# Optimization experiments

Hardware: AMD Instinct MI355X
Metric: run time of the kernel (lower is better)

The kernel has to match this reference:

```python
import jax, jax.numpy as jnp
import numpy as np

MAX_CLUSTERS = 5
CLUSTER_SIZE_MAX = 3
K_HOP = 2
TAU = 1.0  # epoch=0 -> tau_init * decay^0 = 1.0
NEG = -1e9


def _logits(x, ctx, W1, b1, W2, b2):
    # x: [B,N,D], ctx: [B,H] -> logits [B,N] (selection_mlp, dropout=eval/identity)
    B, N, _ = x.shape
    h = jnp.concatenate([x, jnp.broadcast_to(ctx[:, None, :], (B, N, ctx.shape[-1]))], axis=-1)
    h = jax.nn.relu(h @ W1.T + b1)
    return (h @ W2.T + b2)[..., 0]


def _select(logits, cand, key):
    # Hard Gumbel-Softmax argmax over candidate nodes; zeros row if no candidates.
    any_c = cand.any(axis=-1, keepdims=True)
    ml = jnp.where(cand, logits, NEG)
    u = jax.random.uniform(key, logits.shape, dtype=logits.dtype)
    g = -jnp.log(-jnp.log(u + 1e-8) + 1e-8)
    idx = jnp.argmax((ml + g) / TAU, axis=-1)
    oh = jax.nn.one_hot(idx, logits.shape[-1], dtype=logits.dtype)
    return oh * any_c.astype(logits.dtype)


def _gru(seq, h0, Wih, Whh, bih, bhh):
    # torch nn.GRU single layer, batch_first; seq: [B,T,D], h0: [B,H] -> final hidden [B,H]
    def cell(h, xt):
        gi = xt @ Wih.T + bih
        gh = h @ Whh.T + bhh
        ir, iz, inn = jnp.split(gi, 3, axis=-1)
        hr, hz, hn = jnp.split(gh, 3, axis=-1)
        r = jax.nn.sigmoid(ir + hr)
        z = jax.nn.sigmoid(iz + hz)
        n = jnp.tanh(inn + r * hn)
        return (1.0 - z) * n + z * h, None
    h, _ = jax.lax.scan(cell, h0, jnp.swapaxes(seq, 0, 1))
    return h


def reference(x, adj, mask, W1, b1, W2, b2, Wc, bc, Wih, Whh, bih, bhh):
    B, N, D = x.shape
    key = jax.random.key(42)
    avail = mask.astype(bool)
    ctx = x.mean(axis=1) @ Wc.T + bc          # context_init  [B,H]
    h_gru = jnp.zeros_like(ctx)               # context_hidden
    assign = jnp.zeros((B, N, MAX_CLUSTERS), x.dtype)
    embs, hist = [], []
    for c in range(MAX_CLUSTERS):
        # logits are identical for every selection within this cluster (same x, same context)
        logits = _logits(x, ctx, W1, b1, W2, b2)  # [B,N]
        # seed selection (torch uses .item() -> selection is a constant index; no grad path)
        seed = jax.lax.stop_gradient(_select(logits, avail, jax.random.fold_in(key, 2 * c)))
        avail = avail & ~(seed > 0.5)
        # k-hop BFS from seed via adjacency matvecs
        reach = seed > 0.5
        cur = seed
        for _ in range(K_HOP):
            nb = jnp.einsum('bn,bnm->bm', cur, adj) > 0
            new = nb & ~reach
            reach = reach | nb
            cur = new.astype(x.dtype)
        member = seed
        for a in range(CLUSTER_SIZE_MAX - 1):
            cand = avail & reach
            sel = jax.lax.stop_gradient(_select(logits, cand, jax.random.fold_in(key, 2 * c + 1000 + a)))
            avail = avail & ~(sel > 0.5)
            member = member + sel
        assign = assign.at[:, :, c].set(member)
        cnt = member.sum(axis=-1, keepdims=True)
        emb = jnp.einsum('bn,bnd->bd', member, x) / jnp.maximum(cnt, 1.0)  # mean of member feats; 0 if empty
        embs.append(emb)
        hist.append(emb)
        # torch re-runs the GRU over the FULL cluster history each iteration, starting
        # from the previously updated hidden state (faithful to the original code)
        h_gru = _gru(jnp.stack(hist, axis=1), h_gru, Wih, Whh, bih, bhh)
        ctx = h_gru
    cluster_features = jnp.stack(embs, axis=1)               # [B,S,D]
    S = MAX_CLUSTERS
    cluster_adj = jnp.ones((B, S, S), x.dtype) - jnp.eye(S, dtype=x.dtype)[None]
    return cluster_features, cluster_adj, assign


def setup_inputs() -> dict:
    key = jax.random.key(0)
    ks = jax.random.split(key, 10)
    B, N, D, H = 16, 2048, 128, 64
    x = jax.random.normal(ks[0], (B, N, D), dtype=jnp.float32)
    # sparse symmetric binary adjacency, ~16 neighbors per node
    a = (jax.random.uniform(ks[1], (B, N, N)) < 0.004).astype(jnp.float32)
    adj = jnp.clip(a + jnp.swapaxes(a, 1, 2), 0.0, 1.0)
    adj = adj * (1.0 - jnp.eye(N, dtype=jnp.float32)[None])
    mask = jnp.ones((B, N), dtype=jnp.int32)
    s = 0.05
    return {
        'x': x, 'adj': adj, 'mask': mask,
        'W1': jax.random.normal(ks[2], (H, D + H)) * s, 'b1': jnp.zeros((H,)),
        'W2': jax.random.normal(ks[3], (1, H)) * s, 'b2': jnp.zeros((1,)),
        'Wc': jax.random.normal(ks[4], (H, D)) * s, 'bc': jnp.zeros((H,)),
        'Wih': jax.random.normal(ks[5], (3 * H, D)) * s,
        'Whh': jax.random.normal(ks[6], (3 * H, H)) * s,
        'bih': jnp.zeros((3 * H,)), 'bhh': jnp.zeros((3 * H,)),
    }
```

## Files before the change

kernel.cpp:

```cpp
#include <hip/hip_runtime.h>
#include <cfloat>
#include <cmath>

#define NB 2048
#define BB 16
#define DD 128
#define HH 64
#define MAXC 5
#define CSMAX 3
#define NT 1024

__device__ __forceinline__ unsigned rotl32(unsigned v, int d) {
  return (v << d) | (v >> (32 - d));
}

__device__ __forceinline__ void tf2x32(unsigned k0, unsigned k1, unsigned x0, unsigned x1,
                                       unsigned& o0, unsigned& o1) {
  unsigned ks2 = k0 ^ k1 ^ 0x1BD11BDAu;
  x0 += k0; x1 += k1;
#define RND(r) { x0 += x1; x1 = rotl32(x1, r); x1 ^= x0; }
  RND(13) RND(15) RND(26) RND(6)   x0 += k1;  x1 += ks2 + 1u;
  RND(17) RND(29) RND(16) RND(24)  x0 += ks2; x1 += k0 + 2u;
  RND(13) RND(15) RND(26) RND(6)   x0 += k0;  x1 += k1 + 3u;
  RND(17) RND(29) RND(16) RND(24)  x0 += k1;  x1 += ks2 + 4u;
  RND(13) RND(15) RND(26) RND(6)   x0 += ks2; x1 += k0 + 5u;
#undef RND
  o0 = x0; o1 = x1;
}

__device__ __forceinline__ float gumbel_for(unsigned k0, unsigned k1, unsigned idx) {
  unsigned o0, o1;
  tf2x32(k0, k1, 0u, idx, o0, o1);
  unsigned bits = o0 ^ o1;
  float u = __uint_as_float((bits >> 9) | 0x3f800000u) - 1.0f;
  float uu = u + 1e-8f;
  return -logf(-logf(uu) + 1e-8f);
}

__global__ __launch_bounds__(NT) void gvp_prep(
    const float* __restrict__ x, const float* __restrict__ W1,
    float* __restrict__ P, float* __restrict__ partial, float* __restrict__ gumb) {
  __shared__ __align__(16) float s_W1[HH][DD + 4];
  __shared__ float sp[8][DD];
  const int bid = blockIdx.x, tid = threadIdx.x;

  if (bid < 128) {
    for (int i = tid; i < HH * (DD / 4); i += NT) {
      int r = i >> 5, q = i & 31;
      *(float4*)&s_W1[r][q * 4] = *(const float4*)(W1 + (size_t)r * (DD + HH) + q * 4);
    }
    __syncthreads();
    const int jg = tid & 15, ng = tid >> 4;
    const int j0 = jg * 4;
    const size_t n0 = (size_t)bid * 256 + ng * 4;
    const float4* x4 = (const float4*)x;
    float acc[4][4];
#pragma unroll
    for (int i = 0; i < 4; i++)
#pragma unroll
      for (int q = 0; q < 4; q++) acc[i][q] = 0.f;
    for (int kq = 0; kq < 32; kq++) {
      float4 xv[4], wv[4];
#pragma unroll
      for (int i = 0; i < 4; i++) xv[i] = x4[(n0 + i) * 32 + kq];
#pragma unroll
      for (int q = 0; q < 4; q++) wv[q] = *(const float4*)&s_W1[j0 + q][kq * 4];
#pragma unroll
      for (int i = 0; i < 4; i++)
#pragma unroll
        for (int q = 0; q < 4; q++)
          acc[i][q] += xv[i].x * wv[q].x + xv[i].y * wv[q].y +
                       xv[i].z * wv[q].z + xv[i].w * wv[q].w;
    }
#pragma unroll
    for (int i = 0; i < 4; i++)
#pragma unroll
      for (int q = 0; q < 4; q++)
        P[(n0 + i) * HH + j0 + q] = acc[i][q];
  } else if (bid < 384) {
    const int bm = bid - 128;
    const int b = bm >> 4, chunk = bm & 15;
    const int d = tid & (DD - 1), part = tid >> 7;
    float acc = 0.f;
    const int base = chunk * 128 + part;
#pragma unroll
    for (int k = 0; k < 16; k++)
      acc += x[((size_t)b * NB + base + k * 8) * DD + d];
    sp[part][d] = acc;
    __syncthreads();
    if (tid < DD) {
      float m = 0.f;
#pragma unroll
      for (int p = 0; p < 8; p++) m += sp[p][tid];
      partial[((size_t)b * 16 + chunk) * DD + tid] = m;
    }
  } else {
    const int bg = bid - 384;
    const int base = (bg * NT + tid) * 4;
#pragma unroll
    for (int i = 0; i < 4; i++) {
      int idx = base + i;
      int sel = idx >> 15;
      int rem = idx & 32767;
      int c = sel / 3, s = sel - 3 * c;
      unsigned data = (s == 0) ? (unsigned)(2 * c) : (unsigned)(2 * c + 1000 + (s - 1));
      unsigned k0, k1;
      tf2x32(0u, 42u, 0u, data, k0, k1);
      gumb[idx] = gumbel_for(k0, k1, (unsigned)rem);
    }
  }
}

__global__ __launch_bounds__(NT, 4) void gvp_main(
    const float* __restrict__ x, const float* __restrict__ adj, const int* __restrict__ mask,
    const float* __restrict__ W1, const float* __restrict__ b1,
    const float* __restrict__ W2, const float* __restrict__ b2,
    const float* __restrict__ Wc, const float* __restrict__ bc,
    const float* __restrict__ Wih, const float* __restrict__ Whh,
    const float* __restrict__ bih, const float* __restrict__ bhh,
    const float* __restrict__ P, const float* __restrict__ partial,
    const float* __restrict__ gumb,
    float* __restrict__ out_feat, float* __restrict__ out_adjm, float* __restrict__ out_assign) {
  const int b = blockIdx.x;
  const int tid = threadIdx.x;

  __shared__ __align__(16) float s_logits[NB];
  __shared__ __align__(16) float s_gumb[2][NB];
  __shared__ unsigned char s_avail[NB], s_reach[NB], s_assignB[NB];
  __shared__ short s_list[128];
  __shared__ int s_cnt;
  __shared__ unsigned long long s_key[CSMAX];
  __shared__ __align__(16) float s_ctx[HH], s_q[HH];
  __shared__ __align__(16) float s_h[2][HH];
  __shared__ __align__(16) float s_hist[MAXC][DD];
  __shared__ __align__(16) float s_giAll[MAXC][3 * HH];
  __shared__ __align__(16) float s_Whh[3 * HH][HH + 4];
  __shared__ __align__(16) float s_W1c[HH][HH + 4];
  __shared__ __align__(16) float s_W2[HH];
  __shared__ float s_bhh[3 * HH], s_b1[HH];
  __shared__ __align__(16) float s_mean[DD];
  __shared__ float s_b2v;

  const size_t xb = (size_t)b * NB * DD;
  const float4* adj4 = (const float4*)(adj + (size_t)b * NB * NB);
  const float4* P4 = (const float4*)(P + (size_t)b * NB * HH);

  auto scanReduce = [&](float bv, int bi, int slot) {
#pragma unroll
    for (int off = 32; off; off >>= 1) {
      float ov = __shfl_down(bv, off);
      int oi = __shfl_down(bi, off);
      if (ov > bv || (ov == bv && oi < bi)) { bv = ov; bi = oi; }
    }
    if ((tid & 63) == 0 && bi < NB) {
      unsigned u = __float_as_uint(bv);
      u = (u & 0x80000000u) ? ~u : (u | 0x80000000u);
      unsigned long long key = ((unsigned long long)u << 32) | (unsigned)(~bi);
      atomicMax(&s_key[slot], key);
    }
  };
  auto decodeIdx = [](unsigned long long k) -> int {
    return k ? (int)(unsigned)(~(unsigned)k) : -1;
  };

  for (int i = tid; i < 3 * HH * (HH / 4); i += NT) {
    int r = i >> 4, q = i & 15;
    *(float4*)&s_Whh[r][q * 4] = *(const float4*)(Whh + (size_t)r * HH + q * 4);
  }
  {
    int r = tid >> 4, q = tid & 15;
    *(float4*)&s_W1c[r][q * 4] = *(const float4*)(W1 + (size_t)r * (DD + HH) + DD + q * 4);
  }
  if (tid < 3 * HH) s_bhh[tid] = bhh[tid];
  if (tid < HH) { s_W2[tid] = W2[tid]; s_b1[tid] = b1[tid]; s_h[0][tid] = 0.f; }
  if (tid == 0) s_b2v = b2[0];
#pragma unroll
  for (int r = 0; r < 2; r++) {
    int n = tid + r * NT;
    s_avail[n] = (mask[b * NB + n] != 0) ? 1 : 0;
    s_assignB[n] = 0;
  }
  if (tid < DD) {
    float m = 0.f;
#pragma unroll
    for (int k = 0; k < 16; k++) m += partial[((size_t)b * 16 + k) * DD + tid];
    s_mean[tid] = m * (1.0f / NB);
  }
  __syncthreads();
  if (tid < 4 * HH) {
    int row = tid >> 2, g = tid & 3;
    const float4* wr = (const float4*)(Wc + (size_t)row * DD) + g * 8;
    const float4* m4 = (const float4*)s_mean + g * 8;
    float s = 0.f;
#pragma unroll
    for (int i = 0; i < 8; i++) {
      float4 w = wr[i], m = m4[i];
      s += w.x * m.x + w.y * m.y + w.z * m.z + w.w * m.w;
    }
    s += __shfl_xor(s, 1);
    s += __shfl_xor(s, 2);
    if (g == 0) s_ctx[row] = s + bc[row];
  }
  __syncthreads();

  int hp = 0;

  for (int c = 0; c < MAXC; c++) {
    const float* g0p = gumb + ((size_t)(c * 3) * BB + b) * NB;
    const float4* g12 = (const float4*)(gumb + ((size_t)(c * 3 + 1 + (tid >> 9)) * BB + b) * NB);
    float4 gst = g12[tid & 511];
    const int n0 = tid, n1 = tid + NT;
    float gs0 = g0p[n0], gs1 = g0p[n1];
    ((float4*)s_gumb)[tid] = gst;
    if (tid < 4 * HH) {
      int row = tid >> 2, g = tid & 3;
      const float4* wr = (const float4*)&s_W1c[row][0] + g * 4;
      const float4* c4 = (const float4*)s_ctx + g * 4;
      float s = 0.f;
#pragma unroll
      for (int i = 0; i < 4; i++) {
        float4 w = wr[i], cc = c4[i];
        s += w.x * cc.x + w.y * cc.y + w.z * cc.z + w.w * cc.w;
      }
      s += __shfl_xor(s, 1);
      s += __shfl_xor(s, 2);
      if (g == 0) s_q[row] = s + s_b1[row];
    }
    if (tid < CSMAX) s_key[tid] = 0ull;
    if (tid == 0) s_cnt = 0;
    __syncthreads();

    {
      float l0 = s_b2v, l1 = s_b2v;
      const float4* p0 = P4 + (size_t)n0 * 16;
      const float4* p1 = P4 + (size_t)n1 * 16;
      const float4* q4 = (const float4*)s_q;
      const float4* w4 = (const float4*)s_W2;
#pragma unroll
      for (int qq = 0; qq < 16; qq += 4) {
        float4 A[4], Bv[4];
#pragma unroll
        for (int i = 0; i < 4; i++) { A[i] = p0[qq + i]; Bv[i] = p1[qq + i]; }
#pragma unroll
        for (int i = 0; i < 4; i++) {
          float4 qv = q4[qq + i], w = w4[qq + i];
          l0 += w.x * fmaxf(A[i].x + qv.x, 0.f) + w.y * fmaxf(A[i].y + qv.y, 0.f) +
                w.z * fmaxf(A[i].z + qv.z, 0.f) + w.w * fmaxf(A[i].w + qv.w, 0.f);
          l1 += w.x * fmaxf(Bv[i].x + qv.x, 0.f) + w.y * fmaxf(Bv[i].y + qv.y, 0.f) +
                w.z * fmaxf(Bv[i].z + qv.z, 0.f) + w.w * fmaxf(Bv[i].w + qv.w, 0.f);
        }
      }
      s_logits[n0] = l0;
      s_logits[n1] = l1;
      float bv = -FLT_MAX;
      int bi = NB;
      if (s_avail[n0]) { float y = l0 + gs0; if (y > bv) { bv = y; bi = n0; } }
      if (s_avail[n1]) { float y = l1 + gs1; if (y > bv || (y == bv && n1 < bi)) { bv = y; bi = n1; } }
      scanReduce(bv, bi, 0);
    }
    __syncthreads();

    const int seed = decodeIdx(s_key[0]);
    if (tid < 512) {
      if (seed >= 0) {
        float4 a = adj4[(size_t)seed * 512 + tid];
        int m = tid << 2;
        unsigned f0 = a.x > 0.f, f1 = a.y > 0.f, f2 = a.z > 0.f, f3 = a.w > 0.f;
        unsigned r = f0 | (f1 << 8) | (f2 << 16) | (f3 << 24);
        if ((seed >> 2) == tid) r |= 1u << ((seed & 3) * 8);
        ((unsigned*)s_reach)[tid] = r;
        if (f0 && m != seed)     { int p = atomicAdd(&s_cnt, 1); if (p < 128) s_list[p] = (short)m; }
        if (f1 && m + 1 != seed) { int p = atomicAdd(&s_cnt, 1); if (p < 128) s_list[p] = (short)(m + 1); }
        if (f2 && m + 2 != seed) { int p = atomicAdd(&s_cnt, 1); if (p < 128) s_list[p] = (short)(m + 2); }
        if (f3 && m + 3 != seed) { int p = atomicAdd(&s_cnt, 1); if (p < 128) s_list[p] = (short)(m + 3); }
      } else {
        ((unsigned*)s_reach)[tid] = 0u;
      }
    }
    __syncthreads();

    if (seed >= 0) {
      int cnt = min(s_cnt, 128);
      int m4 = tid & 511, rg = tid >> 9;
      bool a0 = false, a1 = false, a2 = false, a3 = false;
#pragma unroll
      for (int k = 0; k < 20; k++) {
        int li = rg + 2 * k;
        if (li < cnt) {
          int n = s_list[li];
          float4 a = adj4[(size_t)n * 512 + m4];
          a0 |= a.x > 0.f; a1 |= a.y > 0.f; a2 |= a.z > 0.f; a3 |= a.w > 0.f;
        }
      }
      for (int li = rg + 40; li < cnt; li += 2) {
        int n = s_list[li];
        float4 a = adj4[(size_t)n * 512 + m4];
        a0 |= a.x > 0.f; a1 |= a.y > 0.f; a2 |= a.z > 0.f; a3 |= a.w > 0.f;
      }
      int m = m4 << 2;
      if (a0) s_reach[m] = 1;
      if (a1) s_reach[m + 1] = 1;
      if (a2) s_reach[m + 2] = 1;
      if (a3) s_reach[m + 3] = 1;
    }
    __syncthreads();

    {
      float bv = -FLT_MAX;
      int bi = NB;
#pragma unroll
      for (int r = 0; r < 2; r++) {
        int n = tid + r * NT;
        if (s_avail[n] && s_reach[n] && n != seed) {
          float y = s_logits[n] + s_gumb[0][n];
          if (y > bv || (y == bv && n < bi)) { bv = y; bi = n; }
        }
      }
      scanReduce(bv, bi, 1);
    }
    __syncthreads();

    const int w1i = decodeIdx(s_key[1]);
    {
      float bv = -FLT_MAX;
      int bi = NB;
#pragma unroll
      for (int r = 0; r < 2; r++) {
        int n = tid + r * NT;
        if (s_avail[n] && s_reach[n] && n != seed && n != w1i) {
          float y = s_logits[n] + s_gumb[1][n];
          if (y > bv || (y == bv && n < bi)) { bv = y; bi = n; }
        }
      }
      scanReduce(bv, bi, 2);
    }
    __syncthreads();

    const int w2i = decodeIdx(s_key[2]);
    {
      int mc = (seed >= 0) + (w1i >= 0) + (w2i >= 0);
      if (tid < DD) {
        float acc = 0.f;
        if (seed >= 0) acc += x[xb + (size_t)seed * DD + tid];
        if (w1i >= 0) acc += x[xb + (size_t)w1i * DD + tid];
        if (w2i >= 0) acc += x[xb + (size_t)w2i * DD + tid];
        float e = acc / fmaxf((float)mc, 1.0f);
        s_hist[c][tid] = e;
        out_feat[((size_t)b * MAXC + c) * DD + tid] = e;
      } else if (tid >= 128 && tid < 128 + CSMAX) {
        int idx = (tid == 128) ? seed : (tid == 129 ? w1i : w2i);
        if (idx >= 0) { s_avail[idx] = 0; s_assignB[idx] |= (unsigned char)(1 << c); }
      }
    }
    __syncthreads();

    if (tid < 4 * 3 * HH) {
      int row = tid >> 2, g = tid & 3;
      const float4* wr = (const float4*)(Wih + (size_t)row * DD) + g * 8;
      const float4* h4 = (const float4*)s_hist[c] + g * 8;
      float s = 0.f;
#pragma unroll
      for (int i = 0; i < 8; i++) {
        float4 w = wr[i], hh = h4[i];
        s += w.x * hh.x + w.y * hh.y + w.z * hh.z + w.w * hh.w;
      }
      s += __shfl_xor(s, 1);
      s += __shfl_xor(s, 2);
      if (g == 0) s_giAll[c][row] = s + bih[row];
    }
    __syncthreads();

    for (int t0 = 0; t0 <= c; t0++) {
      if (tid < 4 * HH) {
        int row = tid >> 2, g = tid & 3;
        const float4* h4 = (const float4*)s_h[hp] + g * 4;
        float4 hv[4];
#pragma unroll
        for (int i = 0; i < 4; i++) hv[i] = h4[i];
        const float4* wr = (const float4*)&s_Whh[row][0] + g * 4;
        const float4* wz = (const float4*)&s_Whh[HH + row][0] + g * 4;
        const float4* wn = (const float4*)&s_Whh[2 * HH + row][0] + g * 4;
        float sr = 0.f, sz = 0.f, sn = 0.f;
#pragma unroll
        for (int i = 0; i < 4; i++) {
          float4 a = wr[i], bz = wz[i], cn = wn[i], h = hv[i];
          sr += a.x * h.x + a.y * h.y + a.z * h.z + a.w * h.w;
          sz += bz.x * h.x + bz.y * h.y + bz.z * h.z + bz.w * h.w;
          sn += cn.x * h.x + cn.y * h.y + cn.z * h.z + cn.w * h.w;
        }
        sr += __shfl_xor(sr, 1); sr += __shfl_xor(sr, 2);
        sz += __shfl_xor(sz, 1); sz += __shfl_xor(sz, 2);
        sn += __shfl_xor(sn, 1); sn += __shfl_xor(sn, 2);
        if (g == 0) {
          float r = 1.f / (1.f + expf(-(s_giAll[t0][row] + sr + s_bhh[row])));
          float z = 1.f / (1.f + expf(-(s_giAll[t0][HH + row] + sz + s_bhh[HH + row])));
          float nn = tanhf(s_giAll[t0][2 * HH + row] + r * (sn + s_bhh[2 * HH + row]));
          float hn = (1.f - z) * nn + z * s_h[hp][row];
          s_h[hp ^ 1][row] = hn;
          if (t0 == c) s_ctx[row] = hn;
        }
      }
      hp ^= 1;
      __syncthreads();
    }
  }

#pragma unroll
  for (int r = 0; r < 2; r++) {
    int n = tid + r * NT;
    unsigned bits = s_assignB[n];
    size_t base = ((size_t)(b * NB + n)) * MAXC;
#pragma unroll
    for (int cc = 0; cc < MAXC; cc++)
      out_assign[base + cc] = (float)((bits >> cc) & 1u);
  }
  for (int i = tid; i < MAXC * MAXC; i += NT)
    out_adjm[(size_t)b * MAXC * MAXC + i] = ((i / MAXC) == (i % MAXC)) ? 0.f : 1.f;
}

extern "C" void kernel_launch(void* const* d_in, const int* in_sizes, int n_in,
                              void* d_out, int out_size, void* d_ws, size_t ws_size,
                              hipStream_t stream) {
  const float* x   = (const float*)d_in[0];
  const float* adj = (const float*)d_in[1];
  const int*   mask= (const int*)d_in[2];
  const float* W1  = (const float*)d_in[3];
  const float* b1  = (const float*)d_in[4];
  const float* W2  = (const float*)d_in[5];
  const float* b2  = (const float*)d_in[6];
  const float* Wc  = (const float*)d_in[7];
  const float* bc  = (const float*)d_in[8];
  const float* Wih = (const float*)d_in[9];
  const float* Whh = (const float*)d_in[10];
  const float* bih = (const float*)d_in[11];
  const float* bhh = (const float*)d_in[12];

  float* ws = (float*)d_ws;
  float* P       = ws;
  float* partial = P + (size_t)BB * NB * HH;
  float* gumb    = partial + (size_t)BB * 16 * DD;

  float* out = (float*)d_out;
  float* out_feat = out;
  float* out_adjm = out + (size_t)BB * MAXC * DD;
  float* out_assign = out_adjm + (size_t)BB * MAXC * MAXC;

  hipLaunchKernelGGL(gvp_prep, dim3(504), dim3(NT), 0, stream, x, W1, P, partial, gumb);
  hipLaunchKernelGGL(gvp_main, dim3(BB), dim3(NT), 0, stream,
                     x, adj, mask, W1, b1, W2, b2, Wc, bc, Wih, Whh, bih, bhh, P, partial, gumb,
                     out_feat, out_adjm, out_assign);
}
```

Baseline: 195.0 us.

## Split each batch across 8 cooperating blocks with global atomic barriers

The main kernel now runs 8 blocks per batch element, each owning a 256-node slice. Each block keeps its slice of P in shared memory and computes Gumbel noise inline instead of reading a precomputed buffer. Cross-block argmax goes through 64-bit packed-key atomicMax, with a top-2 merge for the second pick, and blocks synchronise through a spin barrier on a global counter. This targets the serial per-batch latency of a 16-block launch. In exchange it adds inter-block barrier overhead, redundant GRU work in every block, and relies on all 128 blocks being co-resident.

```diff
diff --git a/kernel.cpp b/kernel.cpp
--- a/kernel.cpp
+++ b/kernel.cpp
@@ -7,8 +7,16 @@
 #define DD 128
 #define HH 64
 #define MAXC 5
-#define CSMAX 3
-#define NT 1024
+#define BPB 8
+#define SLICE 256
+#define MT 512
+
+#define OFF_P 0
+#define OFF_PART (OFF_P + BB * NB * HH)
+#define OFF_SYNC (OFF_PART + BB * 16 * DD)
+#define OFF_K0 (OFF_SYNC + 16)
+#define OFF_K1 (OFF_K0 + BB * MAXC * 2)
+#define OFF_K2 (OFF_K1 + BB * MAXC * 2)
 
 __device__ __forceinline__ unsigned rotl32(unsigned v, int d) {
   return (v << d) | (v >> (32 - d));
@@ -37,15 +45,25 @@
   return -logf(-logf(uu) + 1e-8f);
 }
 
-__global__ __launch_bounds__(NT) void gvp_prep(
-    const float* __restrict__ x, const float* __restrict__ W1,
-    float* __restrict__ P, float* __restrict__ partial, float* __restrict__ gumb) {
+__device__ __forceinline__ unsigned long long packKey(float y, int n) {
+  unsigned u = __float_as_uint(y);
+  u = (u & 0x80000000u) ? ~u : (u | 0x80000000u);
+  return ((unsigned long long)u << 32) | (unsigned)(~(unsigned)n);
+}
+__device__ __forceinline__ int decodeKey(unsigned long long k) {
+  return k ? (int)(~(unsigned)k) : -1;
+}
+
+__global__ __launch_bounds__(1024) void gvp_prep(
+    const float* __restrict__ x, const float* __restrict__ W1, float* __restrict__ ws) {
   __shared__ __align__(16) float s_W1[HH][DD + 4];
   __shared__ float sp[8][DD];
   const int bid = blockIdx.x, tid = threadIdx.x;
+  float* P = ws + OFF_P;
+  float* partial = ws + OFF_PART;
 
   if (bid < 128) {
-    for (int i = tid; i < HH * (DD / 4); i += NT) {
+    for (int i = tid; i < HH * (DD / 4); i += 1024) {
       int r = i >> 5, q = i & 31;
       *(float4*)&s_W1[r][q * 4] = *(const float4*)(W1 + (size_t)r * (DD + HH) + q * 4);
     }
@@ -95,97 +113,179 @@
       partial[((size_t)b * 16 + chunk) * DD + tid] = m;
     }
   } else {
-    const int bg = bid - 384;
-    const int base = (bg * NT + tid) * 4;
-#pragma unroll
-    for (int i = 0; i < 4; i++) {
-      int idx = base + i;
-      int sel = idx >> 15;
-      int rem = idx & 32767;
-      int c = sel / 3, s = sel - 3 * c;
-      unsigned data = (s == 0) ? (unsigned)(2 * c) : (unsigned)(2 * c + 1000 + (s - 1));
-      unsigned k0, k1;
-      tf2x32(0u, 42u, 0u, data, k0, k1);
-      gumb[idx] = gumbel_for(k0, k1, (unsigned)rem);
-    }
-  }
-}
-
-__global__ __launch_bounds__(NT, 4) void gvp_main(
+    int nz = 16 + BB * MAXC * 2 + BB * MAXC * 2;
+    if (tid < nz) ws[OFF_SYNC + tid] = 0.f;
+  }
+}
+
+__global__ __launch_bounds__(MT) void gvp_main(
     const float* __restrict__ x, const float* __restrict__ adj, const int* __restrict__ mask,
     const float* __restrict__ W1, const float* __restrict__ b1,
     const float* __restrict__ W2, const float* __restrict__ b2,
     const float* __restrict__ Wc, const float* __restrict__ bc,
     const float* __restrict__ Wih, const float* __restrict__ Whh,
     const float* __restrict__ bih, const float* __restrict__ bhh,
-    const float* __restrict__ P, const float* __restrict__ partial,
-    const float* __restrict__ gumb,
+    float* __restrict__ ws,
     float* __restrict__ out_feat, float* __restrict__ out_adjm, float* __restrict__ out_assign) {
-  const int b = blockIdx.x;
+  const int gb = blockIdx.x;
+  const int b = gb >> 3, blk = gb & 7;
+  const int base = blk * SLICE;
   const int tid = threadIdx.x;
 
-  __shared__ __align__(16) float s_logits[NB];
-  __shared__ __align__(16) float s_gumb[2][NB];
-  __shared__ unsigned char s_avail[NB], s_reach[NB], s_assignB[NB];
-  __shared__ short s_list[128];
+  __shared__ __align__(16) float s_P[SLICE][HH + 4];
+  __shared__ __align__(16) float s_Whh[3 * HH][HH + 4];
+  __shared__ __align__(16) float s_W1c[HH][HH + 4];
+  __shared__ __align__(16) float s_logits[SLICE];
+  __shared__ unsigned char s_avail[SLICE], s_reach[SLICE], s_assignB[SLICE];
+  __shared__ short s_flist[128];
   __shared__ int s_cnt;
-  __shared__ unsigned long long s_key[CSMAX];
-  __shared__ __align__(16) float s_ctx[HH], s_q[HH];
-  __shared__ __align__(16) float s_h[2][HH];
   __shared__ __align__(16) float s_hist[MAXC][DD];
   __shared__ __align__(16) float s_giAll[MAXC][3 * HH];
-  __shared__ __align__(16) float s_Whh[3 * HH][HH + 4];
-  __shared__ __align__(16) float s_W1c[HH][HH + 4];
-  __shared__ __align__(16) float s_W2[HH];
-  __shared__ float s_bhh[3 * HH], s_b1[HH];
-  __shared__ __align__(16) float s_mean[DD];
+  __shared__ __align__(16) float s_h[2][HH];
+  __shared__ __align__(16) float s_mean[DD], s_ctx[HH], s_q[HH];
+  __shared__ float sp[4][DD];
+  __shared__ float s_bih[3 * HH], s_bhh[3 * HH], s_b1[HH], s_W2[HH];
   __shared__ float s_b2v;
-
+  __shared__ unsigned long long s_redk[8], s_t2r[8][2], s_mrg[17], s_m0;
+
+  unsigned* cnt = (unsigned*)(ws + OFF_SYNC) + b;
+  unsigned long long* K0 = (unsigned long long*)(ws + OFF_K0) + b * MAXC;
+  unsigned long long* K1 = (unsigned long long*)(ws + OFF_K1) + b * MAXC;
+  unsigned long long* K2 = (unsigned long long*)(ws + OFF_K2);
   const size_t xb = (size_t)b * NB * DD;
-  const float4* adj4 = (const float4*)(adj + (size_t)b * NB * NB);
-  const float4* P4 = (const float4*)(P + (size_t)b * NB * HH);
-
-  auto scanReduce = [&](float bv, int bi, int slot) {
+  int bar = 0;
+  int hp = 0;
+
+  auto barrier = [&]() {
+    __threadfence();
+    __syncthreads();
+    ++bar;
+    if (tid == 0) {
+      __hip_atomic_fetch_add(cnt, 1u, __ATOMIC_RELEASE, __HIP_MEMORY_SCOPE_AGENT);
+      while (__hip_atomic_load(cnt, __ATOMIC_ACQUIRE, __HIP_MEMORY_SCOPE_AGENT) <
+             (unsigned)(BPB * bar))
+        __builtin_amdgcn_s_sleep(1);
+    }
+    __syncthreads();
+  };
+
+  auto qFromCtx = [&]() {
+    if (tid < 4 * HH) {
+      int row = tid >> 2, g = tid & 3;
+      const float4* wr = (const float4*)&s_W1c[row][0] + g * 4;
+      const float4* c4 = (const float4*)s_h[hp] + g * 4;
+      float s = 0.f;
+#pragma unroll
+      for (int i = 0; i < 4; i++) {
+        float4 w = wr[i], cc = c4[i];
+        s += w.x * cc.x + w.y * cc.y + w.z * cc.z + w.w * cc.w;
+      }
+      s += __shfl_xor(s, 1);
+      s += __shfl_xor(s, 2);
+      if (g == 0) s_q[row] = s + s_b1[row];
+    }
+  };
+
+  auto gruStep = [&](int t) {
+    if (tid < 4 * HH) {
+      int row = tid >> 2, g = tid & 3;
+      const float4* h4 = (const float4*)s_h[hp] + g * 4;
+      float4 hv[4];
+#pragma unroll
+      for (int i = 0; i < 4; i++) hv[i] = h4[i];
+      const float4* wr = (const float4*)&s_Whh[row][0] + g * 4;
+      const float4* wz = (const float4*)&s_Whh[HH + row][0] + g * 4;
+      const float4* wn = (const float4*)&s_Whh[2 * HH + row][0] + g * 4;
+      float sr = 0.f, sz = 0.f, sn = 0.f;
+#pragma unroll
+      for (int i = 0; i < 4; i++) {
+        float4 a = wr[i], bz = wz[i], cn = wn[i], h = hv[i];
+        sr += a.x * h.x + a.y * h.y + a.z * h.z + a.w * h.w;
+        sz += bz.x * h.x + bz.y * h.y + bz.z * h.z + bz.w * h.w;
+        sn += cn.x * h.x + cn.y * h.y + cn.z * h.z + cn.w * h.w;
+      }
+      sr += __shfl_xor(sr, 1); sr += __shfl_xor(sr, 2);
+      sz += __shfl_xor(sz, 1); sz += __shfl_xor(sz, 2);
+      sn += __shfl_xor(sn, 1); sn += __shfl_xor(sn, 2);
+      if (g == 0) {
+        float r = 1.f / (1.f + expf(-(s_giAll[t][row] + sr + s_bhh[row])));
+        float z = 1.f / (1.f + expf(-(s_giAll[t][HH + row] + sz + s_bhh[HH + row])));
+        float nn = tanhf(s_giAll[t][2 * HH + row] + r * (sn + s_bhh[2 * HH + row]));
+        s_h[hp ^ 1][row] = (1.f - z) * nn + z * s_h[hp][row];
+      }
+    }
+  };
+
+  auto logitsSel0 = [&](int cc) {
+    unsigned ka, kb;
+    tf2x32(0u, 42u, 0u, (unsigned)(2 * cc), ka, kb);
+    int node = tid >> 1, sub = tid & 1;
+    const float4* pr = (const float4*)&s_P[node][0] + sub * 8;
+    const float4* q4 = (const float4*)s_q + sub * 8;
+    const float4* w4 = (const float4*)s_W2 + sub * 8;
+    float l = 0.f;
+#pragma unroll
+    for (int i = 0; i < 8; i++) {
+      float4 p = pr[i], qv = q4[i], w = w4[i];
+      l += w.x * fmaxf(p.x + qv.x, 0.f) + w.y * fmaxf(p.y + qv.y, 0.f) +
+           w.z * fmaxf(p.z + qv.z, 0.f) + w.w * fmaxf(p.w + qv.w, 0.f);
+    }
+    l += __shfl_xor(l, 1);
+    l += s_b2v;
+    unsigned long long key = 0ull;
+    if (sub == 0) {
+      s_logits[node] = l;
+      if (s_avail[node]) {
+        float y = l + gumbel_for(ka, kb, (unsigned)(b * NB + base + node));
+        key = packKey(y, base + node);
+      }
+    }
 #pragma unroll
     for (int off = 32; off; off >>= 1) {
-      float ov = __shfl_down(bv, off);
-      int oi = __shfl_down(bi, off);
-      if (ov > bv || (ov == bv && oi < bi)) { bv = ov; bi = oi; }
-    }
-    if ((tid & 63) == 0 && bi < NB) {
-      unsigned u = __float_as_uint(bv);
-      u = (u & 0x80000000u) ? ~u : (u | 0x80000000u);
-      unsigned long long key = ((unsigned long long)u << 32) | (unsigned)(~bi);
-      atomicMax(&s_key[slot], key);
+      unsigned long long o = __shfl_down(key, off);
+      key = o > key ? o : key;
+    }
+    if ((tid & 63) == 0) s_redk[tid >> 6] = key;
+    __syncthreads();
+    if (tid == 0) {
+      unsigned long long m = s_redk[0];
+#pragma unroll
+      for (int i = 1; i < 8; i++) m = s_redk[i] > m ? s_redk[i] : m;
+      if (m) atomicMax(&K0[cc], m);
     }
   };
-  auto decodeIdx = [](unsigned long long k) -> int {
-    return k ? (int)(unsigned)(~(unsigned)k) : -1;
-  };
-
-  for (int i = tid; i < 3 * HH * (HH / 4); i += NT) {
+
+  {
+    const float4* P4 = (const float4*)(ws + OFF_P);
+    for (int i = tid; i < SLICE * 16; i += MT) {
+      int node = i >> 4, q = i & 15;
+      *(float4*)&s_P[node][q * 4] = P4[(size_t)(b * NB + base + node) * 16 + q];
+    }
+  }
+  for (int i = tid; i < 3 * HH * 16; i += MT) {
     int r = i >> 4, q = i & 15;
     *(float4*)&s_Whh[r][q * 4] = *(const float4*)(Whh + (size_t)r * HH + q * 4);
   }
+  for (int i = tid; i < HH * 16; i += MT) {
+    int r = i >> 4, q = i & 15;
+    *(float4*)&s_W1c[r][q * 4] = *(const float4*)(W1 + (size_t)r * (DD + HH) + DD + q * 4);
+  }
+  if (tid < 3 * HH) { s_bih[tid] = bih[tid]; s_bhh[tid] = bhh[tid]; }
+  if (tid < HH) { s_b1[tid] = b1[tid]; s_W2[tid] = W2[tid]; s_h[0][tid] = 0.f; }
+  if (tid < SLICE) {
+    s_avail[tid] = (mask[b * NB + base + tid] != 0) ? 1 : 0;
+    s_assignB[tid] = 0;
+  }
+  if (tid == 0) s_b2v = b2[0];
   {
-    int r = tid >> 4, q = tid & 15;
-    *(float4*)&s_W1c[r][q * 4] = *(const float4*)(W1 + (size_t)r * (DD + HH) + DD + q * 4);
-  }
-  if (tid < 3 * HH) s_bhh[tid] = bhh[tid];
-  if (tid < HH) { s_W2[tid] = W2[tid]; s_b1[tid] = b1[tid]; s_h[0][tid] = 0.f; }
-  if (tid == 0) s_b2v = b2[0];
-#pragma unroll
-  for (int r = 0; r < 2; r++) {
-    int n = tid + r * NT;
-    s_avail[n] = (mask[b * NB + n] != 0) ? 1 : 0;
-    s_assignB[n] = 0;
-  }
-  if (tid < DD) {
-    float m = 0.f;
-#pragma unroll
-    for (int k = 0; k < 16; k++) m += partial[((size_t)b * 16 + k) * DD + tid];
-    s_mean[tid] = m * (1.0f / NB);
-  }
+    int d = tid & (DD - 1), p = tid >> 7;
+    float a = 0.f;
+    for (int k = p; k < 16; k += 4) a += ws[OFF_PART + ((size_t)b * 16 + k) * DD + d];
+    sp[p][d] = a;
+  }
+  __syncthreads();
+  if (tid < DD)
+    s_mean[tid] = (sp[0][tid] + sp[1][tid] + sp[2][tid] + sp[3][tid]) * (1.0f / NB);
   __syncthreads();
   if (tid < 4 * HH) {
     int row = tid >> 2, g = tid & 3;
@@ -199,223 +299,193 @@
     }
     s += __shfl_xor(s, 1);
     s += __shfl_xor(s, 2);
-    if (g == 0) s_ctx[row] = s + bc[row];
+    if (g == 0) { s_ctx[row] = s + bc[row]; s_h[0][row] = 0.f; }
   }
   __syncthreads();
-
-  int hp = 0;
+  if (tid < 4 * HH) {
+    int row = tid >> 2, g = tid & 3;
+    const float4* wr = (const float4*)&s_W1c[row][0] + g * 4;
+    const float4* c4 = (const float4*)s_ctx + g * 4;
+    float s = 0.f;
+#pragma unroll
+    for (int i = 0; i < 4; i++) {
+      float4 w = wr[i], cc = c4[i];
+      s += w.x * cc.x + w.y * cc.y + w.z * cc.z + w.w * cc.w;
+    }
+    s += __shfl_xor(s, 1);
+    s += __shfl_xor(s, 2);
+    if (g == 0) s_q[row] = s + s_b1[row];
+  }
+  __syncthreads();
+  logitsSel0(0);
+  barrier();
 
   for (int c = 0; c < MAXC; c++) {
-    const float* g0p = gumb + ((size_t)(c * 3) * BB + b) * NB;
-    const float4* g12 = (const float4*)(gumb + ((size_t)(c * 3 + 1 + (tid >> 9)) * BB + b) * NB);
-    float4 gst = g12[tid & 511];
-    const int n0 = tid, n1 = tid + NT;
-    float gs0 = g0p[n0], gs1 = g0p[n1];
-    ((float4*)s_gumb)[tid] = gst;
-    if (tid < 4 * HH) {
-      int row = tid >> 2, g = tid & 3;
-      const float4* wr = (const float4*)&s_W1c[row][0] + g * 4;
-      const float4* c4 = (const float4*)s_ctx + g * 4;
-      float s = 0.f;
-#pragma unroll
-      for (int i = 0; i < 4; i++) {
-        float4 w = wr[i], cc = c4[i];
-        s += w.x * cc.x + w.y * cc.y + w.z * cc.z + w.w * cc.w;
-      }
-      s += __shfl_xor(s, 1);
-      s += __shfl_xor(s, 2);
-      if (g == 0) s_q[row] = s + s_b1[row];
-    }
-    if (tid < CSMAX) s_key[tid] = 0ull;
-    if (tid == 0) s_cnt = 0;
-    __syncthreads();
-
+    if (tid == 0) {
+      s_cnt = 0;
+      s_m0 = __hip_atomic_load(&K0[c], __ATOMIC_ACQUIRE, __HIP_MEMORY_SCOPE_AGENT);
+    }
+    if (tid < SLICE) s_reach[tid] = 0;
+    __syncthreads();
+    const int seed = decodeKey(s_m0);
+    if (tid == 0 && seed >= base && seed < base + SLICE) s_avail[seed - base] = 0;
+    if (seed >= 0) {
+      float4 a = *(const float4*)(adj + ((size_t)b * NB + seed) * NB + tid * 4);
+      int col = tid * 4;
+#pragma unroll
+      for (int e = 0; e < 4; e++) {
+        float v = (e == 0) ? a.x : (e == 1) ? a.y : (e == 2) ? a.z : a.w;
+        if (v > 0.f) {
+          int cg = col + e;
+          if (cg >= base && cg < base + SLICE) s_reach[cg - base] = 1;
+          int p = atomicAdd(&s_cnt, 1);
+          if (p < 128) s_flist[p] = (short)cg;
+        }
+      }
+      if (tid == 0 && seed >= base && seed < base + SLICE) s_reach[seed - base] = 1;
+    }
+    __syncthreads();
+    if (seed >= 0) {
+      int fc = min(s_cnt, 128);
+      int lane = tid & 63;
+      for (int fi = tid >> 6; fi < fc; fi += 8) {
+        int r = s_flist[fi];
+        float4 a = *(const float4*)(adj + ((size_t)b * NB + r) * NB + base + lane * 4);
+        if (a.x > 0.f) s_reach[lane * 4] = 1;
+        if (a.y > 0.f) s_reach[lane * 4 + 1] = 1;
+        if (a.z > 0.f) s_reach[lane * 4 + 2] = 1;
+        if (a.w > 0.f) s_reach[lane * 4 + 3] = 1;
+      }
+    }
+    __syncthreads();
     {
-      float l0 = s_b2v, l1 = s_b2v;
-      const float4* p0 = P4 + (size_t)n0 * 16;
-      const float4* p1 = P4 + (size_t)n1 * 16;
-      const float4* q4 = (const float4*)s_q;
-      const float4* w4 = (const float4*)s_W2;
-#pragma unroll
-      for (int qq = 0; qq < 16; qq += 4) {
-        float4 A[4], Bv[4];
-#pragma unroll
-        for (int i = 0; i < 4; i++) { A[i] = p0[qq + i]; Bv[i] = p1[qq + i]; }
-#pragma unroll
-        for (int i = 0; i < 4; i++) {
-          float4 qv = q4[qq + i], w = w4[qq + i];
-          l0 += w.x * fmaxf(A[i].x + qv.x, 0.f) + w.y * fmaxf(A[i].y + qv.y, 0.f) +
-                w.z * fmaxf(A[i].z + qv.z, 0.f) + w.w * fmaxf(A[i].w + qv.w, 0.f);
-          l1 += w.x * fmaxf(Bv[i].x + qv.x, 0.f) + w.y * fmaxf(Bv[i].y + qv.y, 0.f) +
-                w.z * fmaxf(Bv[i].z + qv.z, 0.f) + w.w * fmaxf(Bv[i].w + qv.w, 0.f);
+      unsigned k1a, k1b, k2a, k2b;
+      tf2x32(0u, 42u, 0u, (unsigned)(2 * c + 1000), k1a, k1b);
+      tf2x32(0u, 42u, 0u, (unsigned)(2 * c + 1001), k2a, k2b);
+      unsigned long long key1 = 0ull, t1 = 0ull, t2 = 0ull;
+      if (tid < SLICE && s_avail[tid] && s_reach[tid]) {
+        unsigned gidx = (unsigned)(b * NB + base + tid);
+        float lg = s_logits[tid];
+        key1 = packKey(lg + gumbel_for(k1a, k1b, gidx), base + tid);
+        t1 = packKey(lg + gumbel_for(k2a, k2b, gidx), base + tid);
+      }
+#pragma unroll
+      for (int off = 32; off; off >>= 1) {
+        unsigned long long o = __shfl_down(key1, off);
+        key1 = o > key1 ? o : key1;
+        unsigned long long o1 = __shfl_down(t1, off);
+        unsigned long long o2 = __shfl_down(t2, off);
+        unsigned long long lo = t1 < o1 ? t1 : o1;
+        unsigned long long hi2 = t2 > o2 ? t2 : o2;
+        t1 = t1 > o1 ? t1 : o1;
+        t2 = lo > hi2 ? lo : hi2;
+      }
+      if ((tid & 63) == 0) {
+        int w = tid >> 6;
+        s_redk[w] = key1;
+        s_t2r[w][0] = t1;
+        s_t2r[w][1] = t2;
+      }
+      __syncthreads();
+      if (tid == 0) {
+        unsigned long long m = 0ull, u1 = 0ull, u2 = 0ull;
+#pragma unroll
+        for (int i = 0; i < 8; i++) {
+          if (s_redk[i] > m) m = s_redk[i];
+          unsigned long long k = s_t2r[i][0];
+          if (k > u1) { u2 = u1; u1 = k; } else if (k > u2) u2 = k;
+          k = s_t2r[i][1];
+          if (k > u1) { u2 = u1; u1 = k; } else if (k > u2) u2 = k;
         }
-      }
-      s_logits[n0] = l0;
-      s_logits[n1] = l1;
-      float bv = -FLT_MAX;
-      int bi = NB;
-      if (s_avail[n0]) { float y = l0 + gs0; if (y > bv) { bv = y; bi = n0; } }
-      if (s_avail[n1]) { float y = l1 + gs1; if (y > bv || (y == bv && n1 < bi)) { bv = y; bi = n1; } }
-      scanReduce(bv, bi, 0);
-    }
-    __syncthreads();
-
-    const int seed = decodeIdx(s_key[0]);
-    if (tid < 512) {
-      if (seed >= 0) {
-        float4 a = adj4[(size_t)seed * 512 + tid];
-        int m = tid << 2;
-        unsigned f0 = a.x > 0.f, f1 = a.y > 0.f, f2 = a.z > 0.f, f3 = a.w > 0.f;
-        unsigned r = f0 | (f1 << 8) | (f2 << 16) | (f3 << 24);
-        if ((seed >> 2) == tid) r |= 1u << ((seed & 3) * 8);
-        ((unsigned*)s_reach)[tid] = r;
-        if (f0 && m != seed)     { int p = atomicAdd(&s_cnt, 1); if (p < 128) s_list[p] = (short)m; }
-        if (f1 && m + 1 != seed) { int p = atomicAdd(&s_cnt, 1); if (p < 128) s_list[p] = (short)(m + 1); }
-        if (f2 && m + 2 != seed) { int p = atomicAdd(&s_cnt, 1); if (p < 128) s_list[p] = (short)(m + 2); }
-        if (f3 && m + 3 != seed) { int p = atomicAdd(&s_cnt, 1); if (p < 128) s_list[p] = (short)(m + 3); }
-      } else {
-        ((unsigned*)s_reach)[tid] = 0u;
-      }
-    }
-    __syncthreads();
-
-    if (seed >= 0) {
-      int cnt = min(s_cnt, 128);
-      int m4 = tid & 511, rg = tid >> 9;
-      bool a0 = false, a1 = false, a2 = false, a3 = false;
-#pragma unroll
-      for (int k = 0; k < 20; k++) {
-        int li = rg + 2 * k;
-        if (li < cnt) {
-          int n = s_list[li];
-          float4 a = adj4[(size_t)n * 512 + m4];
-          a0 |= a.x > 0.f; a1 |= a.y > 0.f; a2 |= a.z > 0.f; a3 |= a.w > 0.f;
-        }
-      }
-      for (int li = rg + 40; li < cnt; li += 2) {
-        int n = s_list[li];
-        float4 a = adj4[(size_t)n * 512 + m4];
-        a0 |= a.x > 0.f; a1 |= a.y > 0.f; a2 |= a.z > 0.f; a3 |= a.w > 0.f;
-      }
-      int m = m4 << 2;
-      if (a0) s_reach[m] = 1;
-      if (a1) s_reach[m + 1] = 1;
-      if (a2) s_reach[m + 2] = 1;
-      if (a3) s_reach[m + 3] = 1;
-    }
-    __syncthreads();
-
+        if (m) atomicMax(&K1[c], m);
+        unsigned long long* slot = K2 + ((size_t)(b * MAXC + c) * BPB + blk) * 2;
+        slot[0] = u1;
+        slot[1] = u2;
+      }
+    }
+    barrier();
+
+    if (tid < 17) {
+      unsigned long long v =
+          (tid == 0)
+              ? __hip_atomic_load(&K1[c], __ATOMIC_ACQUIRE, __HIP_MEMORY_SCOPE_AGENT)
+              : __hip_atomic_load(K2 + (size_t)(b * MAXC + c) * BPB * 2 + tid - 1,
+                                  __ATOMIC_ACQUIRE, __HIP_MEMORY_SCOPE_AGENT);
+      s_mrg[tid] = v;
+    }
+    __syncthreads();
+    const int w1 = decodeKey(s_mrg[0]);
+    int w2;
     {
-      float bv = -FLT_MAX;
-      int bi = NB;
-#pragma unroll
-      for (int r = 0; r < 2; r++) {
-        int n = tid + r * NT;
-        if (s_avail[n] && s_reach[n] && n != seed) {
-          float y = s_logits[n] + s_gumb[0][n];
-          if (y > bv || (y == bv && n < bi)) { bv = y; bi = n; }
-        }
-      }
-      scanReduce(bv, bi, 1);
-    }
-    __syncthreads();
-
-    const int w1i = decodeIdx(s_key[1]);
+      unsigned long long t1 = 0ull, t2 = 0ull;
+#pragma unroll
+      for (int i = 1; i < 17; i++) {
+        unsigned long long k = s_mrg[i];
+        if (k > t1) { t2 = t1; t1 = k; } else if (k > t2) t2 = k;
+      }
+      int i1 = decodeKey(t1);
+      w2 = (i1 == w1) ? decodeKey(t2) : i1;
+    }
+    if (tid == 0) {
+      if (w1 >= base && w1 < base + SLICE) s_avail[w1 - base] = 0;
+      if (w2 >= base && w2 < base + SLICE) s_avail[w2 - base] = 0;
+      if (seed >= base && seed < base + SLICE) s_assignB[seed - base] |= (unsigned char)(1 << c);
+      if (w1 >= base && w1 < base + SLICE) s_assignB[w1 - base] |= (unsigned char)(1 << c);
+      if (w2 >= base && w2 < base + SLICE) s_assignB[w2 - base] |= (unsigned char)(1 << c);
+    }
     {
-      float bv = -FLT_MAX;
-      int bi = NB;
-#pragma unroll
-      for (int r = 0; r < 2; r++) {
-        int n = tid + r * NT;
-        if (s_avail[n] && s_reach[n] && n != seed && n != w1i) {
-          float y = s_logits[n] + s_gumb[1][n];
-          if (y > bv || (y == bv && n < bi)) { bv = y; bi = n; }
-        }
-      }
-      scanReduce(bv, bi, 2);
-    }
-    __syncthreads();
-
-    const int w2i = decodeIdx(s_key[2]);
-    {
-      int mc = (seed >= 0) + (w1i >= 0) + (w2i >= 0);
+      int mc = (seed >= 0) + (w1 >= 0) + (w2 >= 0);
+      float invmc = 1.0f / fmaxf((float)mc, 1.0f);
       if (tid < DD) {
         float acc = 0.f;
         if (seed >= 0) acc += x[xb + (size_t)seed * DD + tid];
-        if (w1i >= 0) acc += x[xb + (size_t)w1i * DD + tid];
-        if (w2i >= 0) acc += x[xb + (size_t)w2i * DD + tid];
-        float e = acc / fmaxf((float)mc, 1.0f);
+        if (w1 >= 0) acc += x[xb + (size_t)w1 * DD + tid];
+        if (w2 >= 0) acc += x[xb + (size_t)w2 * DD + tid];
+        float e = acc * invmc;
         s_hist[c][tid] = e;
-        out_feat[((size_t)b * MAXC + c) * DD + tid] = e;
-      } else if (tid >= 128 && tid < 128 + CSMAX) {
-        int idx = (tid == 128) ? seed : (tid == 129 ? w1i : w2i);
-        if (idx >= 0) { s_avail[idx] = 0; s_assignB[idx] |= (unsigned char)(1 << c); }
-      }
-    }
-    __syncthreads();
-
-    if (tid < 4 * 3 * HH) {
-      int row = tid >> 2, g = tid & 3;
-      const float4* wr = (const float4*)(Wih + (size_t)row * DD) + g * 8;
-      const float4* h4 = (const float4*)s_hist[c] + g * 8;
-      float s = 0.f;
-#pragma unroll
-      for (int i = 0; i < 8; i++) {
-        float4 w = wr[i], hh = h4[i];
-        s += w.x * hh.x + w.y * hh.y + w.z * hh.z + w.w * hh.w;
-      }
-      s += __shfl_xor(s, 1);
-      s += __shfl_xor(s, 2);
-      if (g == 0) s_giAll[c][row] = s + bih[row];
-    }
-    __syncthreads();
-
-    for (int t0 = 0; t0 <= c; t0++) {
-      if (tid < 4 * HH) {
-        int row = tid >> 2, g = tid & 3;
-        const float4* h4 = (const float4*)s_h[hp] + g * 4;
-        float4 hv[4];
-#pragma unroll
-        for (int i = 0; i < 4; i++) hv[i] = h4[i];
-        const float4* wr = (const float4*)&s_Whh[row][0] + g * 4;
-        const float4* wz = (const float4*)&s_Whh[HH + row][0] + g * 4;
-        const float4* wn = (const float4*)&s_Whh[2 * HH + row][0] + g * 4;
-        float sr = 0.f, sz = 0.f, sn = 0.f;
-#pragma unroll
-        for (int i = 0; i < 4; i++) {
-          float4 a = wr[i], bz = wz[i], cn = wn[i], h = hv[i];
-          sr += a.x * h.x + a.y * h.y + a.z * h.z + a.w * h.w;
-          sz += bz.x * h.x + bz.y * h.y + bz.z * h.z + bz.w * h.w;
-          sn += cn.x * h.x + cn.y * h.y + cn.z * h.z + cn.w * h.w;
+        if (blk == 0) out_feat[((size_t)b * MAXC + c) * DD + tid] = e;
+      }
+    }
+    __syncthreads();
+
+    if (c + 1 < MAXC) {
+      if (tid < 2 * 3 * HH) {
+        int row = tid >> 1, half = tid & 1;
+        const float4* wr = (const float4*)(Wih + (size_t)row * DD) + half * 16;
+        const float4* h4 = (const float4*)s_hist[c] + half * 16;
+        float s = 0.f;
+#pragma unroll
+        for (int i = 0; i < 16; i++) {
+          float4 w = wr[i], h = h4[i];
+          s += w.x * h.x + w.y * h.y + w.z * h.z + w.w * h.w;
         }
-        sr += __shfl_xor(sr, 1); sr += __shfl_xor(sr, 2);
-        sz += __shfl_xor(sz, 1); sz += __shfl_xor(sz, 2);
-        sn += __shfl_xor(sn, 1); sn += __shfl_xor(sn, 2);
-        if (g == 0) {
-          float r = 1.f / (1.f + expf(-(s_giAll[t0][row] + sr + s_bhh[row])));
-          float z = 1.f / (1.f + expf(-(s_giAll[t0][HH + row] + sz + s_bhh[HH + row])));
-          float nn = tanhf(s_giAll[t0][2 * HH + row] + r * (sn + s_bhh[2 * HH + row]));
-          float hn = (1.f - z) * nn + z * s_h[hp][row];
-          s_h[hp ^ 1][row] = hn;
-          if (t0 == c) s_ctx[row] = hn;
+        s += __shfl_xor(s, 1);
+        if (half == 0) s_giAll[c][row] = s + s_bih[row];
+      }
+      __syncthreads();
+      for (int t = 0; t <= c; t++) {
+        gruStep(t);
+        hp ^= 1;
+        __syncthreads();
+      }
+      qFromCtx();
+      __syncthreads();
+      logitsSel0(c + 1);
+      barrier();
+    } else {
+      for (int r = tid; r < SLICE * MAXC; r += MT) {
+        int i = r / MAXC, cc = r - MAXC * i;
+        out_assign[((size_t)(b * NB + base + i)) * MAXC + cc] =
+            (float)((s_assignB[i] >> cc) & 1u);
+      }
+      if (gb == 0) {
+        for (int i = tid; i < BB * MAXC * MAXC; i += MT) {
+          int j = i % (MAXC * MAXC);
+          out_adjm[i] = ((j / MAXC) == (j % MAXC)) ? 0.f : 1.f;
         }
       }
-      hp ^= 1;
-      __syncthreads();
-    }
-  }
-
-#pragma unroll
-  for (int r = 0; r < 2; r++) {
-    int n = tid + r * NT;
-    unsigned bits = s_assignB[n];
-    size_t base = ((size_t)(b * NB + n)) * MAXC;
-#pragma unroll
-    for (int cc = 0; cc < MAXC; cc++)
-      out_assign[base + cc] = (float)((bits >> cc) & 1u);
-  }
-  for (int i = tid; i < MAXC * MAXC; i += NT)
-    out_adjm[(size_t)b * MAXC * MAXC + i] = ((i / MAXC) == (i % MAXC)) ? 0.f : 1.f;
+    }
+  }
 }
 
 extern "C" void kernel_launch(void* const* d_in, const int* in_sizes, int n_in,
@@ -436,17 +506,13 @@
   const float* bhh = (const float*)d_in[12];
 
   float* ws = (float*)d_ws;
-  float* P       = ws;
-  float* partial = P + (size_t)BB * NB * HH;
-  float* gumb    = partial + (size_t)BB * 16 * DD;
-
   float* out = (float*)d_out;
   float* out_feat = out;
   float* out_adjm = out + (size_t)BB * MAXC * DD;
   float* out_assign = out_adjm + (size_t)BB * MAXC * MAXC;
 
-  hipLaunchKernelGGL(gvp_prep, dim3(504), dim3(NT), 0, stream, x, W1, P, partial, gumb);
-  hipLaunchKernelGGL(gvp_main, dim3(BB), dim3(NT), 0, stream,
-                     x, adj, mask, W1, b1, W2, b2, Wc, bc, Wih, Whh, bih, bhh, P, partial, gumb,
+  hipLaunchKernelGGL(gvp_prep, dim3(385), dim3(1024), 0, stream, x, W1, ws);
+  hipLaunchKernelGGL(gvp_main, dim3(BB * BPB), dim3(MT), 0, stream,
+                     x, adj, mask, W1, b1, W2, b2, Wc, bc, Wih, Whh, bih, bhh, ws,
                      out_feat, out_adjm, out_assign);
 }
```

New measurement: 295.3 us. 51.5% more time.
